# Kernel tuning notes

Hardware: AMD Instinct MI355X
Metric: run time of the kernel (lower is better)

The kernel has to match this reference:

```python
import jax, jax.numpy as jnp
import numpy as np


def _dct1d_last(x, W_r, W_i):
    """DCT-II along last axis via the even/odd-reorder + FFT trick, ortho norm.

    x: [..., N] real. W_r/W_i: [1, N] rows = cos/sin(-k*pi/(2N)).
    """
    N = x.shape[-1]
    # v = [x[0], x[2], ...] ++ [x[N-1], x[N-3], ..., x[1]]  (torch index/inverted_index)
    v = jnp.concatenate([x[..., 0::2], x[..., 1::2][..., ::-1]], axis=-1)
    Vc = jnp.fft.fft(v, axis=-1)  # complex64
    V = Vc.real * W_r - Vc.imag * W_i  # [..., N]
    # ortho normalization: V[0] /= sqrt(N)*2 ; V[1:] /= sqrt(N/2)*2 ; then V *= 2
    s0 = 1.0 / (np.sqrt(N) * 2.0)
    s1 = 1.0 / (np.sqrt(N / 2.0) * 2.0)
    scale = jnp.concatenate([jnp.full((1,), s0, x.dtype), jnp.full((N - 1,), s1, x.dtype)])
    return 2.0 * V * scale


def setup_inputs() -> dict:
    key = jax.random.key(0)
    H, W = 512, 512
    x = jax.random.normal(key, (32, 3, H, W), dtype=jnp.float32)
    kw = -jnp.arange(W, dtype=jnp.float32)[None, :] * np.pi / (2 * W)
    kh = -jnp.arange(H, dtype=jnp.float32)[None, :] * np.pi / (2 * H)
    return {
        "x": x,
        "W_r_weight": jnp.cos(kw), "W_i_weight": jnp.sin(kw),
        "W_r_height": jnp.cos(kh), "W_i_height": jnp.sin(kh),
    }


def reference(x, W_r_weight, W_i_weight, W_r_height, W_i_height):
    # DCT along width (last axis)
    V = _dct1d_last(x, W_r_weight, W_i_weight)
    # transpose last two dims, DCT along height, transpose back
    V = jnp.swapaxes(V, -1, -2)
    V = _dct1d_last(V, W_r_height, W_i_height)
    return jnp.swapaxes(V, -1, -2)
```

## Files before the change

kernel.cpp:

```cpp
#include <hip/hip_runtime.h>
#include <math.h>

#define NN 512

typedef __attribute__((ext_vector_type(8))) short bf16x8;
typedef __attribute__((ext_vector_type(4))) float f32x4;
typedef __attribute__((ext_vector_type(4))) unsigned int u32x4;

__device__ inline unsigned short f2bf(float f) {
    unsigned u = __builtin_bit_cast(unsigned, f);
    u += 0x7fffu + ((u >> 16) & 1u);
    return (unsigned short)(u >> 16);
}
__device__ inline float bf2f(unsigned short h) {
    unsigned u = ((unsigned)h) << 16;
    return __builtin_bit_cast(float, u);
}
__device__ inline unsigned cvtpk_bf16(float lo, float hi) {
    unsigned r;
    asm("v_cvt_pk_bf16_f32 %0, %1, %2" : "=v"(r) : "v"(lo), "v"(hi));
    return r;
}

__global__ __launch_bounds__(256) void fill_dct_half(unsigned short* __restrict__ Ce,
                                                     unsigned short* __restrict__ Co) {
    int idx = blockIdx.x * 256 + threadIdx.x;
    int par = idx >> 16;
    int kk = (idx >> 8) & 255;
    int n = idx & 255;
    int k = 2 * kk + par;
    int m = ((2 * n + 1) * k) & 2047;
    float ang = (float)m * 3.0679615757712823e-3f;
    float s = (k == 0) ? 0.04419417382415922f : 0.0625f;
    unsigned short v = f2bf(s * cosf(ang));
    if (par) Co[kk * 256 + n] = v; else Ce[kk * 256 + n] = v;
}

#define GLB(p) ((const __attribute__((address_space(1))) unsigned int*)(const void*)(p))
#define LDS(p) ((__attribute__((address_space(3))) unsigned int*)(p))

template <int PASS>
__global__ __launch_bounds__(512, 4) void gemm_dct(const void* __restrict__ Ap,
                                                   const unsigned short* __restrict__ Ce,
                                                   const unsigned short* __restrict__ Cop,
                                                   void* __restrict__ Outp,
                                                   size_t strideIn, size_t strideOut) {
    const int nwg = (int)gridDim.x;
    const int cpx = nwg >> 3;
    const int bid = (int)blockIdx.x;
    const int nid = (bid & 7) * cpx + (bid >> 3);
    const int bx = nid & 3;
    const int by = (nid >> 2) & 3;
    const int bz = nid >> 4;

    __shared__ unsigned short sm[40960];
    unsigned short* const Rs = (PASS == 1) ? sm : sm + 24576;
    unsigned short* const Gs = (PASS == 1) ? sm + 16384 : sm;

    const int t = threadIdx.x;
    const int lane = t & 63;
    const int wave = t >> 6;
    const int wr = wave >> 2;
    const int wc = wave & 3;
    const int lr = lane & 15;
    const int kgx = ((lane >> 4) * 8) ^ (((lr >> 1) & 3) << 3);

    const int srow = t >> 2;
    const int sslot = t & 3;
    const int scol = (sslot ^ ((srow >> 1) & 3)) * 8;

    const int frow = t >> 2;
    const int fq = t & 3;
    const int fslot = (fq ^ ((frow >> 1) & 3)) * 8;

    const float* Xf = nullptr;
    const unsigned short* Tp = nullptr;
    const unsigned short* Gmat;
    int grow0, sgn, row0, col0;
    if constexpr (PASS == 1) {
        Xf = (const float*)Ap + (size_t)bz * strideIn;
        row0 = by * 128;
        col0 = bx * 128;
        Gmat = (bx < 2) ? Ce : Cop; grow0 = (bx & 1) * 128; sgn = (bx >= 2);
    } else {
        Tp = (const unsigned short*)Ap + (size_t)bz * strideIn;
        col0 = bx * 128;
        row0 = 0;
        Gmat = (by < 2) ? Ce : Cop; grow0 = (by & 1) * 128; sgn = (by >= 2);
    }
    const float sgnf = sgn ? -1.0f : 1.0f;

    f32x4 acc[4][2] = {};

    f32x4 rf[2][2], rm[2][2];
    bf16x8 gf[2], gm[2];

    auto stageG = [&](int buf, int k0) {
#pragma unroll
        for (int h = 0; h < 2; ++h)
            __builtin_amdgcn_global_load_lds(
                GLB(Gmat + (size_t)(grow0 + srow) * 256 + k0 + h * 32 + scol),
                LDS(&Gs[buf * 8192 + h * 4096 + srow * 32 + sslot * 8]), 16, 0, 0);
    };
    auto doLR = [&](int k0) {
        if constexpr (PASS == 1) {
#pragma unroll
            for (int h = 0; h < 2; ++h) {
                const float* bfp = Xf + (size_t)(row0 + frow) * NN + k0 + h * 32 + fq * 8;
                const float* bmp = Xf + (size_t)(row0 + frow) * NN + (504 - k0 - h * 32 - fq * 8);
                rf[h][0] = *reinterpret_cast<const f32x4*>(bfp);
                rf[h][1] = *reinterpret_cast<const f32x4*>(bfp + 4);
                rm[h][0] = *reinterpret_cast<const f32x4*>(bmp);
                rm[h][1] = *reinterpret_cast<const f32x4*>(bmp + 4);
            }
        } else {
#pragma unroll
            for (int h = 0; h < 2; ++h) {
                const unsigned short* bfp = Tp + (size_t)(col0 + frow) * NN + k0 + h * 32 + fq * 8;
                const unsigned short* bmp = Tp + (size_t)(col0 + frow) * NN + (504 - k0 - h * 32 - fq * 8);
                gf[h] = *reinterpret_cast<const bf16x8*>(bfp);
                gm[h] = *reinterpret_cast<const bf16x8*>(bmp);
            }
        }
    };
    auto doCW = [&](int s) {
        const int buf = s & 1;
#pragma unroll
        for (int h = 0; h < 2; ++h) {
            unsigned p[4];
            if constexpr (PASS == 1) {
#pragma unroll
                for (int q = 0; q < 4; ++q) {
                    const int j0 = 2 * q, j1 = 2 * q + 1;
                    const int r0 = 7 - j0, r1 = 7 - j1;
                    float s0 = fmaf(sgnf, rm[h][r0 >> 2][r0 & 3], rf[h][j0 >> 2][j0 & 3]);
                    float s1 = fmaf(sgnf, rm[h][r1 >> 2][r1 & 3], rf[h][j1 >> 2][j1 & 3]);
                    p[q] = cvtpk_bf16(s0, s1);
                }
            } else {
#pragma unroll
                for (int q = 0; q < 4; ++q) {
                    const int j0 = 2 * q, j1 = 2 * q + 1;
                    float a0 = bf2f((unsigned short)gf[h][j0]);
                    float a1 = bf2f((unsigned short)gf[h][j1]);
                    float b0 = bf2f((unsigned short)gm[h][7 - j0]);
                    float b1 = bf2f((unsigned short)gm[h][7 - j1]);
                    p[q] = cvtpk_bf16(fmaf(sgnf, b0, a0), fmaf(sgnf, b1, a1));
                }
            }
            u32x4 w = {p[0], p[1], p[2], p[3]};
            *reinterpret_cast<u32x4*>(&Rs[buf * 8192 + h * 4096 + frow * 32 + fslot]) = w;
        }
    };
    auto compute = [&](int kt) {
        const int rofs = (kt & 1) * 8192;
        const int gofs = (kt % 3) * 8192;
        const unsigned short* const Aside = (PASS == 1) ? Rs : Gs;
        const unsigned short* const Bside = (PASS == 1) ? Gs : Rs;
        const int aofs = (PASS == 1) ? rofs : gofs;
        const int bofs = (PASS == 1) ? gofs : rofs;
#pragma unroll
        for (int ks = 0; ks < 2; ++ks) {
            const int ho = ks * 4096;
            bf16x8 a[4], b[2];
#pragma unroll
            for (int mi = 0; mi < 4; ++mi)
                a[mi] = *reinterpret_cast<const bf16x8*>(
                    &Aside[aofs + ho + (wr * 64 + mi * 16 + lr) * 32 + kgx]);
#pragma unroll
            for (int ni = 0; ni < 2; ++ni)
                b[ni] = *reinterpret_cast<const bf16x8*>(
                    &Bside[bofs + ho + (wc * 32 + ni * 16 + lr) * 32 + kgx]);
            __builtin_amdgcn_s_setprio(1);
#pragma unroll
            for (int mi = 0; mi < 4; ++mi)
#pragma unroll
                for (int ni = 0; ni < 2; ++ni)
                    acc[mi][ni] = __builtin_amdgcn_mfma_f32_16x16x32_bf16(a[mi], b[ni],
                                                                          acc[mi][ni], 0, 0, 0);
            __builtin_amdgcn_s_setprio(0);
        }
    };

    stageG(0, 0);
    stageG(1, 64);
    asm volatile("" ::: "memory");
    doLR(0);
    doCW(0);
    doLR(64);
    asm volatile("s_waitcnt lgkmcnt(0)" ::: "memory");
    __builtin_amdgcn_s_barrier();

#pragma unroll
    for (int kt = 0; kt < 4; ++kt) {
        if (kt + 2 <= 3) stageG((kt + 2) % 3, (kt + 2) * 64);
        asm volatile("" ::: "memory");
        if (kt + 1 <= 3) doCW(kt + 1);
        if (kt + 2 <= 3) doLR((kt + 2) * 64);
        compute(kt);
        asm volatile("s_waitcnt lgkmcnt(0)" ::: "memory");
        if (kt < 3) __builtin_amdgcn_s_barrier();
    }

    if constexpr (PASS == 1) {
        unsigned short* T = (unsigned short*)Outp + (size_t)bz * strideOut;
        __builtin_amdgcn_s_barrier();
#pragma unroll
        for (int mi = 0; mi < 4; ++mi)
#pragma unroll
            for (int ni = 0; ni < 2; ++ni) {
                int gr = wr * 64 + mi * 16 + (lane >> 4) * 4;
                int gc = wc * 32 + ni * 16 + lr;
                ushort4 v;
                v.x = f2bf(acc[mi][ni][0]);
                v.y = f2bf(acc[mi][ni][1]);
                v.z = f2bf(acc[mi][ni][2]);
                v.w = f2bf(acc[mi][ni][3]);
                *reinterpret_cast<ushort4*>(&sm[gc * 132 + gr]) = v;
            }
        asm volatile("s_waitcnt lgkmcnt(0)" ::: "memory");
        __builtin_amdgcn_s_barrier();
#pragma unroll
        for (int it = 0; it < 4; ++it) {
            int gcr = wave * 16 + it * 4 + (lane >> 4);
            int physRow = (bx & 1) * 256 + 2 * gcr + (bx >> 1);
            int cb = lr * 8;
            u32x4 d = *reinterpret_cast<const u32x4*>(&sm[gcr * 132 + cb]);
            *reinterpret_cast<u32x4*>(&T[(size_t)physRow * NN + row0 + cb]) = d;
        }
    } else {
        float* O = (float*)Outp + (size_t)bz * strideOut;
#pragma unroll
        for (int mi = 0; mi < 4; ++mi)
#pragma unroll
            for (int ni = 0; ni < 2; ++ni) {
                int gc = col0 + wc * 32 + ni * 16 + lr;
#pragma unroll
                for (int rr = 0; rr < 4; ++rr) {
                    int grl = wr * 64 + mi * 16 + (lane >> 4) * 4 + rr;
                    int ih = (by & 1) * 128 + grl;
                    int q = 2 * ih + (by >> 1);
                    O[(size_t)q * NN + gc] = acc[mi][ni][rr];
                }
            }
    }
}

extern "C" void kernel_launch(void* const* d_in, const int* in_sizes, int n_in,
                              void* d_out, int out_size, void* d_ws, size_t ws_size,
                              hipStream_t stream) {
    const float* x = (const float*)d_in[0];
    float* out = (float*)d_out;

    const int imgs = in_sizes[0] / (NN * NN);
    const size_t imgElems = (size_t)NN * NN;
    const size_t imgB16 = imgElems * 2;

    unsigned short* Ce = (unsigned short*)d_ws;
    unsigned short* Co = Ce + 65536;
    unsigned short* Tb = Co + 65536;

    long long budget = (long long)ws_size - 262144;
    int maxchunk = (int)(budget / (long long)imgB16);
    if (maxchunk < 1) maxchunk = 1;
    if (maxchunk > imgs) maxchunk = imgs;

    hipLaunchKernelGGL(fill_dct_half, dim3(512), dim3(256), 0, stream, Ce, Co);

    for (int i0 = 0; i0 < imgs; i0 += maxchunk) {
        int c = imgs - i0 < maxchunk ? imgs - i0 : maxchunk;
        hipLaunchKernelGGL((gemm_dct<1>), dim3(16 * c), dim3(512), 0, stream,
                           x + (size_t)i0 * imgElems, Ce, Co, Tb, imgElems, imgElems);
        hipLaunchKernelGGL((gemm_dct<2>), dim3(16 * c), dim3(512), 0, stream,
                           Tb, Ce, Co, out + (size_t)i0 * imgElems, imgElems, imgElems);
    }
}
```

Baseline: 69.10 us.

## Enlarge GEMM tile to 128x256 so each block reuses folded input across both halves

Each block now computes a 128x256 output tile, covering the full even- or odd-parity half of the DCT matrix, instead of a 128x128 tile. This halves the grid and the number of times the folded input rows are loaded and converted. Each wave holds 4x4 MFMA accumulators, LDS grows to 128 KB for the triple-buffered matrix tiles, and launch bounds drop to 2 blocks per CU. The cost is lower occupancy, higher register pressure, and fewer blocks to spread across CUs.

```diff
diff --git a/kernel.cpp b/kernel.cpp
--- a/kernel.cpp
+++ b/kernel.cpp
@@ -40,7 +40,7 @@
 #define LDS(p) ((__attribute__((address_space(3))) unsigned int*)(p))
 
 template <int PASS>
-__global__ __launch_bounds__(512, 4) void gemm_dct(const void* __restrict__ Ap,
+__global__ __launch_bounds__(512, 2) void gemm_dct(const void* __restrict__ Ap,
                                                    const unsigned short* __restrict__ Ce,
                                                    const unsigned short* __restrict__ Cop,
                                                    void* __restrict__ Outp,
@@ -49,21 +49,21 @@
     const int cpx = nwg >> 3;
     const int bid = (int)blockIdx.x;
     const int nid = (bid & 7) * cpx + (bid >> 3);
-    const int bx = nid & 3;
-    const int by = (nid >> 2) & 3;
-    const int bz = nid >> 4;
-
-    __shared__ unsigned short sm[40960];
-    unsigned short* const Rs = (PASS == 1) ? sm : sm + 24576;
-    unsigned short* const Gs = (PASS == 1) ? sm + 16384 : sm;
+    const int par = nid & 1;
+    const int bq = (nid >> 1) & 3;
+    const int bz = nid >> 3;
+
+    __shared__ unsigned short sm[65536];
+    unsigned short* const Gs = sm;
+    unsigned short* const Rs = sm + 49152;
 
     const int t = threadIdx.x;
     const int lane = t & 63;
     const int wave = t >> 6;
-    const int wr = wave >> 2;
-    const int wc = wave & 3;
     const int lr = lane & 15;
     const int kgx = ((lane >> 4) * 8) ^ (((lr >> 1) & 3) << 3);
+    const int aw = (PASS == 1) ? (wave >> 2) : (wave >> 1);
+    const int bw = (PASS == 1) ? (wave & 3) : (wave & 1);
 
     const int srow = t >> 2;
     const int sslot = t & 3;
@@ -75,32 +75,32 @@
 
     const float* Xf = nullptr;
     const unsigned short* Tp = nullptr;
-    const unsigned short* Gmat;
-    int grow0, sgn, row0, col0;
+    const unsigned short* const Gmat = par ? Cop : Ce;
+    const float sgnf = par ? -1.0f : 1.0f;
+    int row0 = 0, col0 = 0;
     if constexpr (PASS == 1) {
         Xf = (const float*)Ap + (size_t)bz * strideIn;
-        row0 = by * 128;
-        col0 = bx * 128;
-        Gmat = (bx < 2) ? Ce : Cop; grow0 = (bx & 1) * 128; sgn = (bx >= 2);
+        row0 = bq * 128;
     } else {
         Tp = (const unsigned short*)Ap + (size_t)bz * strideIn;
-        col0 = bx * 128;
-        row0 = 0;
-        Gmat = (by < 2) ? Ce : Cop; grow0 = (by & 1) * 128; sgn = (by >= 2);
-    }
-    const float sgnf = sgn ? -1.0f : 1.0f;
-
-    f32x4 acc[4][2] = {};
+        col0 = bq * 128;
+    }
+
+    f32x4 acc[4][4] = {};
 
     f32x4 rf[2][2], rm[2][2];
     bf16x8 gf[2], gm[2];
 
     auto stageG = [&](int buf, int k0) {
 #pragma unroll
-        for (int h = 0; h < 2; ++h)
-            __builtin_amdgcn_global_load_lds(
-                GLB(Gmat + (size_t)(grow0 + srow) * 256 + k0 + h * 32 + scol),
-                LDS(&Gs[buf * 8192 + h * 4096 + srow * 32 + sslot * 8]), 16, 0, 0);
+        for (int h = 0; h < 2; ++h) {
+#pragma unroll
+            for (int rh = 0; rh < 2; ++rh)
+                __builtin_amdgcn_global_load_lds(
+                    GLB(Gmat + (size_t)(rh * 128 + srow) * 256 + k0 + h * 32 + scol),
+                    LDS(&Gs[buf * 16384 + h * 8192 + (rh * 128 + srow) * 32 + sslot * 8]),
+                    16, 0, 0);
+        }
     };
     auto doLR = [&](int k0) {
         if constexpr (PASS == 1) {
@@ -154,28 +154,34 @@
     };
     auto compute = [&](int kt) {
         const int rofs = (kt & 1) * 8192;
-        const int gofs = (kt % 3) * 8192;
-        const unsigned short* const Aside = (PASS == 1) ? Rs : Gs;
-        const unsigned short* const Bside = (PASS == 1) ? Gs : Rs;
-        const int aofs = (PASS == 1) ? rofs : gofs;
-        const int bofs = (PASS == 1) ? gofs : rofs;
+        const int gofs = (kt % 3) * 16384;
 #pragma unroll
         for (int ks = 0; ks < 2; ++ks) {
-            const int ho = ks * 4096;
-            bf16x8 a[4], b[2];
+            bf16x8 a[4], b[4];
+            if constexpr (PASS == 1) {
+#pragma unroll
+                for (int mi = 0; mi < 4; ++mi)
+                    a[mi] = *reinterpret_cast<const bf16x8*>(
+                        &Rs[rofs + ks * 4096 + (aw * 64 + mi * 16 + lr) * 32 + kgx]);
+#pragma unroll
+                for (int ni = 0; ni < 4; ++ni)
+                    b[ni] = *reinterpret_cast<const bf16x8*>(
+                        &Gs[gofs + ks * 8192 + (bw * 64 + ni * 16 + lr) * 32 + kgx]);
+            } else {
+#pragma unroll
+                for (int mi = 0; mi < 4; ++mi)
+                    a[mi] = *reinterpret_cast<const bf16x8*>(
+                        &Gs[gofs + ks * 8192 + (aw * 64 + mi * 16 + lr) * 32 + kgx]);
+#pragma unroll
+                for (int ni = 0; ni < 4; ++ni)
+                    b[ni] = *reinterpret_cast<const bf16x8*>(
+                        &Rs[rofs + ks * 4096 + (bw * 64 + ni * 16 + lr) * 32 + kgx]);
+            }
+            __builtin_amdgcn_s_setprio(1);
 #pragma unroll
             for (int mi = 0; mi < 4; ++mi)
-                a[mi] = *reinterpret_cast<const bf16x8*>(
-                    &Aside[aofs + ho + (wr * 64 + mi * 16 + lr) * 32 + kgx]);
-#pragma unroll
-            for (int ni = 0; ni < 2; ++ni)
-                b[ni] = *reinterpret_cast<const bf16x8*>(
-                    &Bside[bofs + ho + (wc * 32 + ni * 16 + lr) * 32 + kgx]);
-            __builtin_amdgcn_s_setprio(1);
-#pragma unroll
-            for (int mi = 0; mi < 4; ++mi)
-#pragma unroll
-                for (int ni = 0; ni < 2; ++ni)
+#pragma unroll
+                for (int ni = 0; ni < 4; ++ni)
                     acc[mi][ni] = __builtin_amdgcn_mfma_f32_16x16x32_bf16(a[mi], b[ni],
                                                                           acc[mi][ni], 0, 0, 0);
             __builtin_amdgcn_s_setprio(0);
@@ -208,9 +214,9 @@
 #pragma unroll
         for (int mi = 0; mi < 4; ++mi)
 #pragma unroll
-            for (int ni = 0; ni < 2; ++ni) {
-                int gr = wr * 64 + mi * 16 + (lane >> 4) * 4;
-                int gc = wc * 32 + ni * 16 + lr;
+            for (int ni = 0; ni < 4; ++ni) {
+                int gr = aw * 64 + mi * 16 + (lane >> 4) * 4;
+                int gc = bw * 64 + ni * 16 + lr;
                 ushort4 v;
                 v.x = f2bf(acc[mi][ni][0]);
                 v.y = f2bf(acc[mi][ni][1]);
@@ -221,10 +227,10 @@
         asm volatile("s_waitcnt lgkmcnt(0)" ::: "memory");
         __builtin_amdgcn_s_barrier();
 #pragma unroll
-        for (int it = 0; it < 4; ++it) {
-            int gcr = wave * 16 + it * 4 + (lane >> 4);
-            int physRow = (bx & 1) * 256 + 2 * gcr + (bx >> 1);
-            int cb = lr * 8;
+        for (int it = 0; it < 8; ++it) {
+            int gcr = it * 32 + (t >> 4);
+            int physRow = 2 * gcr + par;
+            int cb = (t & 15) * 8;
             u32x4 d = *reinterpret_cast<const u32x4*>(&sm[gcr * 132 + cb]);
             *reinterpret_cast<u32x4*>(&T[(size_t)physRow * NN + row0 + cb]) = d;
         }
@@ -233,13 +239,12 @@
 #pragma unroll
         for (int mi = 0; mi < 4; ++mi)
 #pragma unroll
-            for (int ni = 0; ni < 2; ++ni) {
-                int gc = col0 + wc * 32 + ni * 16 + lr;
+            for (int ni = 0; ni < 4; ++ni) {
+                int gc = col0 + bw * 64 + ni * 16 + lr;
 #pragma unroll
                 for (int rr = 0; rr < 4; ++rr) {
-                    int grl = wr * 64 + mi * 16 + (lane >> 4) * 4 + rr;
-                    int ih = (by & 1) * 128 + grl;
-                    int q = 2 * ih + (by >> 1);
+                    int qp = aw * 64 + mi * 16 + (lane >> 4) * 4 + rr;
+                    int q = 2 * qp + par;
                     O[(size_t)q * NN + gc] = acc[mi][ni][rr];
                 }
             }
@@ -269,9 +274,9 @@
 
     for (int i0 = 0; i0 < imgs; i0 += maxchunk) {
         int c = imgs - i0 < maxchunk ? imgs - i0 : maxchunk;
-        hipLaunchKernelGGL((gemm_dct<1>), dim3(16 * c), dim3(512), 0, stream,
+        hipLaunchKernelGGL((gemm_dct<1>), dim3(8 * c), dim3(512), 0, stream,
                            x + (size_t)i0 * imgElems, Ce, Co, Tb, imgElems, imgElems);
-        hipLaunchKernelGGL((gemm_dct<2>), dim3(16 * c), dim3(512), 0, stream,
+        hipLaunchKernelGGL((gemm_dct<2>), dim3(8 * c), dim3(512), 0, stream,
                            Tb, Ce, Co, out + (size_t)i0 * imgElems, imgElems, imgElems);
     }
 }
```

After: 78.24 us. 1.13x slower.
